# Performance work log

Measured on AMD Instinct MI355X. Metric: run time of the kernel, lower is better.

## Reference

```python
import jax, jax.numpy as jnp
import numpy as np
import math

D = 2048
NH = 16
DH = D // NH
LAT = D // 4
B, S = 2, 2048
EPS = 1e-5


def _ln(x, g, b):
    m = jnp.mean(x, axis=-1, keepdims=True)
    v = jnp.mean((x - m) ** 2, axis=-1, keepdims=True)
    return (x - m) * jax.lax.rsqrt(v + EPS) * g + b


def setup_inputs() -> dict:
    key = jax.random.key(0)
    ks = jax.random.split(key, 12)
    p = lambda k, shape: 0.01 * jax.random.normal(k, shape, dtype=jnp.float32)
    return {
        "x": jax.random.normal(ks[0], (B, S, D), dtype=jnp.float32),
        "W_dq": p(ks[1], (D, LAT)),
        "W_uq": p(ks[2], (LAT, D)),
        "q_ln_g": jnp.ones((LAT,), jnp.float32),
        "q_ln_b": jnp.zeros((LAT,), jnp.float32),
        "W_dkv": p(ks[3], (D, LAT)),
        "W_ukv": p(ks[4], (LAT, 2 * D)),
        "kv_ln_g": jnp.ones((LAT,), jnp.float32),
        "kv_ln_b": jnp.zeros((LAT,), jnp.float32),
        "W_o": p(ks[5], (D, D)),
        "norm1_g": jnp.ones((D,), jnp.float32),
        "norm1_b": jnp.zeros((D,), jnp.float32),
        "norm2_g": jnp.ones((D,), jnp.float32),
        "norm2_b": jnp.zeros((D,), jnp.float32),
        "fc1_w": p(ks[6], (4 * D, D)),
        "fc1_b": jnp.zeros((4 * D,), jnp.float32),
        "fc2_w": p(ks[7], (D, 4 * D)),
        "fc2_b": jnp.zeros((D,), jnp.float32),
    }


def reference(x, W_dq, W_uq, q_ln_g, q_ln_b, W_dkv, W_ukv, kv_ln_g, kv_ln_b,
              W_o, norm1_g, norm1_b, norm2_g, norm2_b, fc1_w, fc1_b, fc2_w, fc2_b):
    normed = _ln(x, norm1_g, norm1_b)

    # --- RopelessMLA attention ---
    cq = _ln(normed @ W_dq, q_ln_g, q_ln_b)          # [B,S,LAT]
    Q = cq @ W_uq                                     # [B,S,D]
    ckv = _ln(normed @ W_dkv, kv_ln_g, kv_ln_b)       # [B,S,LAT]
    KV = ckv @ W_ukv                                  # [B,S,2D]
    K, V = KV[..., :D], KV[..., D:]

    q = Q.reshape(B, S, NH, DH)
    k = K.reshape(B, S, NH, DH)
    v = V.reshape(B, S, NH, DH)

    qkt = jnp.einsum("bqhd,bkhd->bhqk", q, k) / math.sqrt(float(DH))
    mask = jnp.tril(jnp.ones((S, S), dtype=qkt.dtype))  # causal, past_length=0
    qkt = qkt * mask
    qkt = jnp.where(qkt == 0.0, -jnp.inf, qkt)  # faithful to original zero->-inf trick
    attn = jax.nn.softmax(qkt, axis=-1)
    o = jnp.einsum("bhqk,bkhd->bqhd", attn, v).reshape(B, S, D)
    mh_x = o @ W_o.T

    x = x + mh_x
    h = _ln(x, norm2_g, norm2_b)
    h = jax.nn.relu(h @ fc1_w.T + fc1_b)
    h = h @ fc2_w.T + fc2_b  # dropout is identity in eval mode
    return x + h
```

## Files before the change

kernel.cpp:

```cpp
#include <hip/hip_runtime.h>
#include <hip/hip_bf16.h>


#define DEVI __device__ __forceinline__

typedef __attribute__((ext_vector_type(8))) short bf16x8;
typedef __attribute__((ext_vector_type(4))) float f32x4;

DEVI unsigned short f2bf(float f) {
  union { float f; unsigned u; } v; v.f = f;
  unsigned r = v.u + 0x7fffu + ((v.u >> 16) & 1u);
  return (unsigned short)(r >> 16);
}

DEVI float bf2f(unsigned short u) {
  union { unsigned u; float f; } v; v.u = ((unsigned)u) << 16;
  return v.f;
}

#define GLDS16(gp, lp)                                              \
  __builtin_amdgcn_global_load_lds(                                 \
      (__attribute__((address_space(1))) void*)(gp),                \
      (__attribute__((address_space(3))) void*)(lp), 16, 0, 0)

#define NEG_INF (-__builtin_inff())

__global__ __launch_bounds__(256) void cast_f32_bf16(
    const float* __restrict__ in, unsigned short* __restrict__ out, long n) {
  long i = ((long)blockIdx.x * 256 + threadIdx.x) * 4;
  if (i >= n) return;
  const float4 v = *reinterpret_cast<const float4*>(in + i);
  ushort4 o;
  o.x = f2bf(v.x); o.y = f2bf(v.y); o.z = f2bf(v.z); o.w = f2bf(v.w);
  *reinterpret_cast<ushort4*>(out + i) = o;
}

__global__ __launch_bounds__(256) void transpose_cast(
    const float* __restrict__ in, unsigned short* __restrict__ out, int R, int C) {
  __shared__ float tile[32][33];
  const int c0 = blockIdx.x * 32, r0 = blockIdx.y * 32;
  const int tx = threadIdx.x & 31, ty = threadIdx.x >> 5;
#pragma unroll
  for (int i = 0; i < 32; i += 8)
    tile[ty + i][tx] = in[(long)(r0 + ty + i) * C + c0 + tx];
  __syncthreads();
#pragma unroll
  for (int i = 0; i < 32; i += 8)
    out[(long)(c0 + ty + i) * R + r0 + tx] = f2bf(tile[tx][ty + i]);
}

__global__ __launch_bounds__(256) void v_transpose(
    const unsigned short* __restrict__ KV, unsigned short* __restrict__ Vt) {
  __shared__ unsigned short sh[32][33];
  const int s0 = blockIdx.x * 32, d0 = blockIdx.y * 32, bh = blockIdx.z;
  const int b = bh >> 4, h = bh & 15;
  const int tx = threadIdx.x & 31, ty = threadIdx.x >> 5;
#pragma unroll
  for (int i = 0; i < 32; i += 8)
    sh[ty + i][tx] = KV[((long)(b * 2048 + s0 + ty + i)) * 4096 + 2048 + h * 128 + d0 + tx];
  __syncthreads();
#pragma unroll
  for (int i = 0; i < 32; i += 8)
    Vt[((long)(bh * 128 + d0 + ty + i)) * 2048 + s0 + tx] = sh[tx][ty + i];
}

DEVI float blockReduceSum(float v) {
  v += __shfl_xor(v, 1);  v += __shfl_xor(v, 2);  v += __shfl_xor(v, 4);
  v += __shfl_xor(v, 8);  v += __shfl_xor(v, 16); v += __shfl_xor(v, 32);
  __shared__ float red[4];
  if ((threadIdx.x & 63) == 0) red[threadIdx.x >> 6] = v;
  __syncthreads();
  v = red[0] + red[1] + red[2] + red[3];
  __syncthreads();
  return v;
}

template <int W>
__global__ __launch_bounds__(256) void layernorm_bf16(
    const float* __restrict__ in, const float* __restrict__ g,
    const float* __restrict__ b, unsigned short* __restrict__ out, int ldin) {
  constexpr int VPT = W / 256;
  const long row = blockIdx.x;
  const float* x = in + row * ldin;
  float v[VPT];
  float s = 0.f;
#pragma unroll
  for (int i = 0; i < VPT; i++) { v[i] = x[threadIdx.x + i * 256]; s += v[i]; }
  s = blockReduceSum(s);
  const float mean = s * (1.0f / W);
  float s2 = 0.f;
#pragma unroll
  for (int i = 0; i < VPT; i++) { float d = v[i] - mean; s2 += d * d; }
  s2 = blockReduceSum(s2);
  const float rstd = rsqrtf(s2 * (1.0f / W) + 1e-5f);
#pragma unroll
  for (int i = 0; i < VPT; i++) {
    const int c = threadIdx.x + i * 256;
    out[row * W + c] = f2bf((v[i] - mean) * rstd * g[c] + b[c]);
  }
}

__global__ __launch_bounds__(256) void combine_ln(
    const unsigned short* __restrict__ p, const float* __restrict__ xres,
    const float* __restrict__ g, const float* __restrict__ b,
    float* __restrict__ x2, unsigned short* __restrict__ h1, long n) {
  const int c0 = threadIdx.x * 8;
  const long base = (long)blockIdx.x * 2048 + c0;
  float v[8];
  float s = 0.f;
#pragma unroll
  for (int hh = 0; hh < 2; hh++) {
    const long i = base + hh * 4;
    const ushort4 a  = *reinterpret_cast<const ushort4*>(p + i);
    const ushort4 bb = *reinterpret_cast<const ushort4*>(p + n + i);
    const float4 r = *reinterpret_cast<const float4*>(xres + i);
    float4 o;
    o.x = r.x + bf2f(a.x) + bf2f(bb.x);
    o.y = r.y + bf2f(a.y) + bf2f(bb.y);
    o.z = r.z + bf2f(a.z) + bf2f(bb.z);
    o.w = r.w + bf2f(a.w) + bf2f(bb.w);
    *reinterpret_cast<float4*>(x2 + i) = o;
    v[hh * 4 + 0] = o.x; v[hh * 4 + 1] = o.y;
    v[hh * 4 + 2] = o.z; v[hh * 4 + 3] = o.w;
    s += o.x + o.y + o.z + o.w;
  }
  s = blockReduceSum(s);
  const float mean = s * (1.0f / 2048.f);
  float s2 = 0.f;
#pragma unroll
  for (int i = 0; i < 8; i++) { float d = v[i] - mean; s2 += d * d; }
  s2 = blockReduceSum(s2);
  const float rstd = rsqrtf(s2 * (1.0f / 2048.f) + 1e-5f);
#pragma unroll
  for (int hh = 0; hh < 2; hh++) {
    const float4 gv = *reinterpret_cast<const float4*>(g + c0 + hh * 4);
    const float4 bv = *reinterpret_cast<const float4*>(b + c0 + hh * 4);
    ushort4 o;
    o.x = f2bf((v[hh * 4 + 0] - mean) * rstd * gv.x + bv.x);
    o.y = f2bf((v[hh * 4 + 1] - mean) * rstd * gv.y + bv.y);
    o.z = f2bf((v[hh * 4 + 2] - mean) * rstd * gv.z + bv.z);
    o.w = f2bf((v[hh * 4 + 3] - mean) * rstd * gv.w + bv.w);
    *reinterpret_cast<ushort4*>(h1 + base + hh * 4) = o;
  }
}

template <bool BIAS, bool RELU, bool RES, bool OBF16>
__global__ __launch_bounds__(256) void gemm_bt(
    const unsigned short* __restrict__ A, const unsigned short* __restrict__ Bt,
    const float* __restrict__ bias, const float* __restrict__ res,
    void* __restrict__ Cout, int M, int N, int K) {
  __shared__ __align__(16) unsigned short As[2][128 * 32];
  __shared__ __align__(16) unsigned short Bs[2][128 * 32];

  const int m0 = blockIdx.x * 128;
  const int n0 = blockIdx.y * 128;
  const int tid = threadIdx.x;
  const int lane = tid & 63, w = tid >> 6;
  const int wr = (w >> 1) * 64, wc = (w & 1) * 64;
  const int lrow = lane & 15, lk = (lane >> 4) * 8;

  f32x4 acc[4][4] = {};

  const int nt = K >> 5;
  const int r_ = (tid * 8) >> 5;
  const int c_ = (tid * 8) & 31;

#define STAGE(buf, t)                                                        \
  {                                                                          \
    const long k0 = (long)(t) * 32;                                          \
    GLDS16(A + (long)(m0 + r_) * K + k0 + c_, &As[buf][tid * 8]);            \
    GLDS16(A + (long)(m0 + 64 + r_) * K + k0 + c_, &As[buf][2048 + tid * 8]);\
    GLDS16(Bt + (long)(n0 + r_) * K + k0 + c_, &Bs[buf][tid * 8]);           \
    GLDS16(Bt + (long)(n0 + 64 + r_) * K + k0 + c_, &Bs[buf][2048 + tid * 8]);\
  }

  STAGE(0, 0)
  __syncthreads();
  int cur = 0;
  for (int t = 0; t < nt; t++) {
    if (t + 1 < nt) STAGE(cur ^ 1, t + 1)
    bf16x8 fa[4], fb[4];
#pragma unroll
    for (int i = 0; i < 4; i++) {
      fa[i] = *reinterpret_cast<const bf16x8*>(&As[cur][(wr + i * 16 + lrow) * 32 + lk]);
      fb[i] = *reinterpret_cast<const bf16x8*>(&Bs[cur][(wc + i * 16 + lrow) * 32 + lk]);
    }
#pragma unroll
    for (int i = 0; i < 4; i++)
#pragma unroll
      for (int j = 0; j < 4; j++)
        acc[i][j] = __builtin_amdgcn_mfma_f32_16x16x32_bf16(fa[i], fb[j], acc[i][j], 0, 0, 0);
    __syncthreads();
    cur ^= 1;
  }
#undef STAGE

#pragma unroll
  for (int i = 0; i < 4; i++) {
#pragma unroll
    for (int j = 0; j < 4; j++) {
      const int row = m0 + wr + i * 16 + ((lane >> 4) << 2);
      const int col = n0 + wc + j * 16 + lrow;
      float bv = 0.f;
      if (BIAS) bv = bias[col];
#pragma unroll
      for (int r = 0; r < 4; r++) {
        float v = acc[i][j][r];
        const long idx = (long)(row + r) * N + col;
        if (BIAS) v += bv;
        if (RELU) v = fmaxf(v, 0.f);
        if (RES) v += res[idx];
        if (OBF16) ((unsigned short*)Cout)[idx] = f2bf(v);
        else       ((float*)Cout)[idx] = v;
      }
    }
  }
}

template <bool BIAS, bool RELU, bool OBF16>
__global__ __launch_bounds__(512, 1) void gemm256p(
    const unsigned short* __restrict__ A, const unsigned short* __restrict__ Bt,
    const float* __restrict__ bias, void* __restrict__ Cout,
    int M, int N, int lda, int ldb, int kLen, long kOff) {
  __shared__ __align__(16) unsigned short L[2][2][2][256 * 32];

  const int m0 = blockIdx.x * 256, n0 = blockIdx.y * 256;
  const long ka = (long)blockIdx.z * kOff;
  const int tid = threadIdx.x;
  const int lane = tid & 63, w = tid >> 6;
  const int sr = (w >> 2) * 64, sc = (w & 3) * 32;
  const int g = lane >> 4, lrow = lane & 15;
  const int r_ = tid >> 2, s_ = tid & 3;

  f32x4 acc[2][2][4][2] = {};
  const int nt = kLen >> 6;

#define STG1(bb, ab, h, kh, t, P, base0, ld)                                   \
  {                                                                            \
    const long k0 = ka + (long)(t) * 64 + (kh) * 32;                           \
    const int rr = (h) * 128 + r_;                                             \
    GLDS16((P) + (long)((base0) + rr) * (ld) + k0 + ((s_ ^ ((rr >> 1) & 3)) << 3), \
           &L[bb][ab][kh][((h) * 512 + tid) * 8]);                             \
  }
#define STG_A(bb, h, t) STG1(bb, 0, h, 0, t, A, m0, lda) STG1(bb, 0, h, 1, t, A, m0, lda)
#define STG_B(bb, h, t) STG1(bb, 1, h, 0, t, Bt, n0, ldb) STG1(bb, 1, h, 1, t, Bt, n0, ldb)

#define RD(dst, ab, kh, row)                                                   \
  dst = *reinterpret_cast<const bf16x8*>(                                      \
      &L[bu][ab][kh][((row) * 4 + (g ^ (((row) >> 1) & 3))) * 8]);

#define PH_READS(a, b)                                                         \
  bf16x8 fa[2][4], fb[2][2];                                                   \
  _Pragma("unroll")                                                            \
  for (int kh = 0; kh < 2; kh++) {                                             \
    _Pragma("unroll")                                                          \
    for (int i = 0; i < 4; i++) {                                              \
      const int rr = (a) * 128 + sr + i * 16 + lrow;                           \
      RD(fa[kh][i], 0, kh, rr)                                                 \
    }                                                                          \
    _Pragma("unroll")                                                          \
    for (int j = 0; j < 2; j++) {                                              \
      const int rr = (b) * 128 + sc + j * 16 + lrow;                           \
      RD(fb[kh][j], 1, kh, rr)                                                 \
    }                                                                          \
  }

#define PH_MFMA(a, b)                                                          \
  __builtin_amdgcn_s_setprio(1);                                               \
  _Pragma("unroll")                                                            \
  for (int kh = 0; kh < 2; kh++)                                               \
    _Pragma("unroll")                                                          \
    for (int i = 0; i < 4; i++)                                                \
      _Pragma("unroll")                                                        \
      for (int j = 0; j < 2; j++)                                              \
        acc[a][b][i][j] = __builtin_amdgcn_mfma_f32_16x16x32_bf16(             \
            fa[kh][i], fb[kh][j], acc[a][b][i][j], 0, 0, 0);                   \
  __builtin_amdgcn_s_setprio(0);

  STG_A(0, 0, 0) STG_B(0, 0, 0) STG_A(0, 1, 0) STG_B(0, 1, 0)
  asm volatile("s_waitcnt vmcnt(0)\n\ts_barrier" ::: "memory");

  int t = 0;
  for (; t < nt - 1; t++) {
    const int bu = t & 1, bn = bu ^ 1;
    {
      PH_READS(0, 0)
      STG_A(bn, 0, t + 1)
      PH_MFMA(0, 0)
      asm volatile("s_waitcnt vmcnt(4)\n\ts_barrier" ::: "memory");
    }
    {
      PH_READS(1, 0)
      STG_B(bn, 0, t + 1)
      PH_MFMA(1, 0)
      asm volatile("s_waitcnt vmcnt(4)\n\ts_barrier" ::: "memory");
    }
    {
      PH_READS(1, 1)
      STG_A(bn, 1, t + 1)
      PH_MFMA(1, 1)
    }
    {
      PH_READS(0, 1)
      STG_B(bn, 1, t + 1)
      PH_MFMA(0, 1)
      asm volatile("s_waitcnt vmcnt(4)\n\ts_barrier" ::: "memory");
    }
  }
  {
    const int bu = t & 1;
    {
      PH_READS(0, 0)
      PH_MFMA(0, 0)
      asm volatile("s_waitcnt vmcnt(2)\n\ts_barrier" ::: "memory");
    }
    {
      PH_READS(1, 0)
      PH_MFMA(1, 0)
      asm volatile("s_waitcnt vmcnt(0)\n\ts_barrier" ::: "memory");
    }
    {
      PH_READS(1, 1)
      PH_MFMA(1, 1)
    }
    {
      PH_READS(0, 1)
      PH_MFMA(0, 1)
    }
  }
#undef STG1
#undef STG_A
#undef STG_B
#undef RD
#undef PH_READS
#undef PH_MFMA

  const long zoff = (long)blockIdx.z * (long)M * (long)N;
#pragma unroll
  for (int a = 0; a < 2; a++) {
#pragma unroll
    for (int b = 0; b < 2; b++) {
#pragma unroll
      for (int i = 0; i < 4; i++) {
#pragma unroll
        for (int j = 0; j < 2; j++) {
          const int row = m0 + a * 128 + sr + i * 16 + g * 4;
          const int col = n0 + b * 128 + sc + j * 16 + lrow;
          float bv = 0.f;
          if (BIAS) bv = bias[col];
#pragma unroll
          for (int r = 0; r < 4; r++) {
            float v = acc[a][b][i][j][r];
            if (BIAS) v += bv;
            if (RELU) v = fmaxf(v, 0.f);
            const long idx = zoff + (long)(row + r) * N + col;
            if (OBF16) ((unsigned short*)Cout)[idx] = f2bf(v);
            else       ((float*)Cout)[idx] = v;
          }
        }
      }
    }
  }
}

template <bool BIAS>
__global__ __launch_bounds__(256) void combine2(
    const unsigned short* __restrict__ p, const float* __restrict__ bias,
    const float* __restrict__ res, float* __restrict__ out, long n) {
  const long i = ((long)blockIdx.x * 256 + threadIdx.x) * 4;
  if (i >= n) return;
  const ushort4 a = *reinterpret_cast<const ushort4*>(p + i);
  const ushort4 b = *reinterpret_cast<const ushort4*>(p + n + i);
  const float4 r = *reinterpret_cast<const float4*>(res + i);
  float4 o;
  o.x = bf2f(a.x) + bf2f(b.x) + r.x;
  o.y = bf2f(a.y) + bf2f(b.y) + r.y;
  o.z = bf2f(a.z) + bf2f(b.z) + r.z;
  o.w = bf2f(a.w) + bf2f(b.w) + r.w;
  if (BIAS) {
    const int col = (int)(i & 2047);
    const float4 bv = *reinterpret_cast<const float4*>(bias + col);
    o.x += bv.x; o.y += bv.y; o.z += bv.z; o.w += bv.w;
  }
  *reinterpret_cast<float4*>(out + i) = o;
}

__global__ __launch_bounds__(256) void flash_attn(
    const unsigned short* __restrict__ Q, const unsigned short* __restrict__ KV,
    const unsigned short* __restrict__ Vt, unsigned short* __restrict__ O) {
  constexpr int S = 2048;
  const int tid = threadIdx.x, lane = tid & 63, w = tid >> 6;
  const int g = lane >> 4, lcol = lane & 15;
  const int wg = blockIdx.x;
  const int x8 = wg & 7, q64 = wg >> 3;
  const int p = q64 & 15, hi = q64 >> 4;
  const int bh = x8 * 4 + hi;
  const int b = bh >> 4, h = bh & 15;
  const long kvrow0 = (long)b * S;
  const int hd0 = h * 128;

  __shared__ __align__(16) unsigned short Kl[64 * 128];
  __shared__ __align__(16) unsigned short Vl[128 * 64];
  __shared__ __align__(16) unsigned short Pl[4 * 16 * 72];

  const float kscale = 0.08838834764831845f * 1.4426950408889634f;

  for (int ti = 0; ti < 2; ti++) {
    const int t = ti ? (31 - p) : p;
    const int qbase = t * 64;
    bf16x8 qf[4];
#pragma unroll
    for (int dc = 0; dc < 4; dc++)
      qf[dc] = *reinterpret_cast<const bf16x8*>(
          Q + (kvrow0 + qbase + w * 16 + lcol) * 2048 + hd0 + dc * 32 + g * 8);
    f32x4 oacc[8] = {};
    float mst[4] = {NEG_INF, NEG_INF, NEG_INF, NEG_INF};
    float lst[4] = {0.f, 0.f, 0.f, 0.f};
    const int nk = t + 1;
    for (int kt = 0; kt < nk; kt++) {
      const int kv0 = kt * 64;
      __syncthreads();
#pragma unroll
      for (int i = 0; i < 4; i++) {
        const int o16 = i * 256 + tid;
        const int kr = o16 >> 4, ks = o16 & 15;
        GLDS16(KV + (kvrow0 + kv0 + kr) * 4096 + hd0 + 8 * (ks ^ (kr & 7)),
               Kl + o16 * 8);
        const int vd = o16 >> 3, vs = o16 & 7;
        GLDS16(Vt + ((long)bh * 128 + vd) * 2048 + kv0 + 8 * (vs ^ (vd & 7)),
               Vl + o16 * 8);
      }
      __syncthreads();
      f32x4 sc[4] = {};
      __builtin_amdgcn_s_setprio(1);
#pragma unroll
      for (int dc = 0; dc < 4; dc++) {
#pragma unroll
        for (int c = 0; c < 4; c++) {
          const bf16x8 kf = *reinterpret_cast<const bf16x8*>(
              Kl + (c * 16 + lcol) * 128 + 8 * ((4 * dc + g) ^ (lcol & 7)));
          sc[c] = __builtin_amdgcn_mfma_f32_16x16x32_bf16(qf[dc], kf, sc[c], 0, 0, 0);
        }
      }
      __builtin_amdgcn_s_setprio(0);
      float s[4][4];
      const int qrow = qbase + w * 16 + g * 4;
      if (kt == nk - 1) {
#pragma unroll
        for (int c = 0; c < 4; c++) {
          const int col = kv0 + c * 16 + lcol;
#pragma unroll
          for (int r = 0; r < 4; r++)
            s[c][r] = (col <= qrow + r) ? sc[c][r] * kscale : NEG_INF;
        }
      } else {
#pragma unroll
        for (int c = 0; c < 4; c++)
#pragma unroll
          for (int r = 0; r < 4; r++) s[c][r] = sc[c][r] * kscale;
      }
      float pm[4];
#pragma unroll
      for (int r = 0; r < 4; r++) {
        float mx = fmaxf(fmaxf(s[0][r], s[1][r]), fmaxf(s[2][r], s[3][r]));
        mx = fmaxf(mx, __shfl_xor(mx, 1));
        mx = fmaxf(mx, __shfl_xor(mx, 2));
        mx = fmaxf(mx, __shfl_xor(mx, 4));
        mx = fmaxf(mx, __shfl_xor(mx, 8));
        pm[r] = mx;
      }
      bool need = false;
#pragma unroll
      for (int r = 0; r < 4; r++) need = need || (pm[r] > mst[r] + 11.5f);
      if (__any(need)) {
#pragma unroll
        for (int r = 0; r < 4; r++) {
          const float mnew = fmaxf(mst[r], pm[r]);
          const float corr = exp2f(mst[r] - mnew);
          mst[r] = mnew;
          lst[r] *= corr;
#pragma unroll
          for (int db = 0; db < 8; db++) oacc[db][r] *= corr;
        }
      }
#pragma unroll
      for (int r = 0; r < 4; r++) {
        float ps = 0.f;
#pragma unroll
        for (int c = 0; c < 4; c++) {
          const float pv = exp2f(s[c][r] - mst[r]);
          Pl[(w * 16 + g * 4 + r) * 72 + c * 16 + lcol] = f2bf(pv);
          ps += pv;
        }
        ps += __shfl_xor(ps, 1); ps += __shfl_xor(ps, 2);
        ps += __shfl_xor(ps, 4); ps += __shfl_xor(ps, 8);
        lst[r] += ps;
      }
      __builtin_amdgcn_s_setprio(1);
#pragma unroll
      for (int kk = 0; kk < 2; kk++) {
        const bf16x8 pf = *reinterpret_cast<const bf16x8*>(
            Pl + (w * 16 + lcol) * 72 + kk * 32 + g * 8);
#pragma unroll
        for (int db = 0; db < 8; db++) {
          const bf16x8 vf = *reinterpret_cast<const bf16x8*>(
              Vl + (db * 16 + lcol) * 64 + 8 * ((4 * kk + g) ^ (lcol & 7)));
          oacc[db] = __builtin_amdgcn_mfma_f32_16x16x32_bf16(pf, vf, oacc[db], 0, 0, 0);
        }
      }
      __builtin_amdgcn_s_setprio(0);
    }
#pragma unroll
    for (int db = 0; db < 8; db++)
#pragma unroll
      for (int r = 0; r < 4; r++) {
        const int qi = qbase + w * 16 + g * 4 + r;
        O[(kvrow0 + qi) * 2048 + hd0 + db * 16 + lcol] = f2bf(oacc[db][r] / lst[r]);
      }
  }
}

extern "C" void kernel_launch(void* const* d_in, const int* in_sizes, int n_in,
                              void* d_out, int out_size, void* d_ws, size_t ws_size,
                              hipStream_t stream) {
  (void)in_sizes; (void)n_in; (void)out_size; (void)ws_size;
  const float* x     = (const float*)d_in[0];
  const float* W_dq  = (const float*)d_in[1];
  const float* W_uq  = (const float*)d_in[2];
  const float* qlng  = (const float*)d_in[3];
  const float* qlnb  = (const float*)d_in[4];
  const float* W_dkv = (const float*)d_in[5];
  const float* W_ukv = (const float*)d_in[6];
  const float* klng  = (const float*)d_in[7];
  const float* klnb  = (const float*)d_in[8];
  const float* W_o   = (const float*)d_in[9];
  const float* n1g   = (const float*)d_in[10];
  const float* n1b   = (const float*)d_in[11];
  const float* n2g   = (const float*)d_in[12];
  const float* n2b   = (const float*)d_in[13];
  const float* fc1w  = (const float*)d_in[14];
  const float* fc1b  = (const float*)d_in[15];
  const float* fc2w  = (const float*)d_in[16];
  const float* fc2b  = (const float*)d_in[17];
  float* out = (float*)d_out;

  char* ws = (char*)d_ws;
  unsigned short* normed = (unsigned short*)(ws + 0);
  unsigned short* Obuf   = (unsigned short*)(ws + 0);
  unsigned short* fc2bb  = (unsigned short*)(ws + 0);
  float*          cqkv_pre = (float*)(ws + 33554432);
  unsigned short* KV       = (unsigned short*)(ws + 33554432);
  unsigned short* fc1bb    = (unsigned short*)(ws + 33554432);
  unsigned short* fc2part  = (unsigned short*)(ws + 33554432);
  unsigned short* cq  = (unsigned short*)(ws + 67108864);
  unsigned short* Qb = (unsigned short*)(ws + 71303168);
  unsigned short* h1 = (unsigned short*)(ws + 71303168);
  unsigned short* ckv = (unsigned short*)(ws + 88080384);
  float* x2           = (float*)(ws + 88080384);
  unsigned short* Vtb    = (unsigned short*)(ws + 121634816);
  unsigned short* wopart = (unsigned short*)(ws + 121634816);
  unsigned short* hmid   = (unsigned short*)(ws + 121634816);
  unsigned short* dqkv_t = (unsigned short*)(ws + 188743680);
  unsigned short* uq_t   = dqkv_t + 2097152;
  unsigned short* ukv_t  = uq_t + 1048576;
  unsigned short* wo_b   = ukv_t + 2097152;

  const dim3 blk(256);
  const dim3 blk8(512);

  transpose_cast<<<dim3(512 / 32, 2048 / 32), blk, 0, stream>>>(W_dq, dqkv_t, 2048, 512);
  transpose_cast<<<dim3(512 / 32, 2048 / 32), blk, 0, stream>>>(W_dkv, dqkv_t + 512 * 2048, 2048, 512);
  transpose_cast<<<dim3(2048 / 32, 512 / 32), blk, 0, stream>>>(W_uq, uq_t, 512, 2048);
  transpose_cast<<<dim3(4096 / 32, 512 / 32), blk, 0, stream>>>(W_ukv, ukv_t, 512, 4096);
  cast_f32_bf16<<<2048 * 2048 / 1024, blk, 0, stream>>>(W_o, wo_b, 2048 * 2048);

  layernorm_bf16<2048><<<4096, blk, 0, stream>>>(x, n1g, n1b, normed, 2048);
  gemm_bt<false, false, false, false><<<dim3(32, 8), blk, 0, stream>>>(
      normed, dqkv_t, nullptr, nullptr, cqkv_pre, 4096, 1024, 2048);
  layernorm_bf16<512><<<4096, blk, 0, stream>>>(cqkv_pre, qlng, qlnb, cq, 1024);
  layernorm_bf16<512><<<4096, blk, 0, stream>>>(cqkv_pre + 512, klng, klnb, ckv, 1024);
  gemm_bt<false, false, false, true><<<dim3(32, 16), blk, 0, stream>>>(
      cq, uq_t, nullptr, nullptr, Qb, 4096, 2048, 512);
  gemm256p<false, false, true><<<dim3(16, 16), blk8, 0, stream>>>(
      ckv, ukv_t, nullptr, KV, 4096, 4096, 512, 512, 512, 0);
  v_transpose<<<dim3(64, 4, 32), blk, 0, stream>>>(KV, Vtb);
  flash_attn<<<dim3(512), blk, 0, stream>>>(Qb, KV, Vtb, Obuf);
  cast_f32_bf16<<<8192 * 2048 / 1024, blk, 0, stream>>>(fc1w, fc1bb, 8192L * 2048);
  gemm256p<false, false, true><<<dim3(16, 8, 2), blk8, 0, stream>>>(
      Obuf, wo_b, nullptr, wopart, 4096, 2048, 2048, 2048, 1024, 1024);
  cast_f32_bf16<<<2048 * 8192 / 1024, blk, 0, stream>>>(fc2w, fc2bb, 2048L * 8192);
  combine_ln<<<4096, blk, 0, stream>>>(wopart, x, n2g, n2b, x2, h1, 8388608L);
  gemm256p<true, true, true><<<dim3(16, 32), blk8, 0, stream>>>(
      h1, fc1bb, fc1b, hmid, 4096, 8192, 2048, 2048, 2048, 0);
  gemm256p<false, false, true><<<dim3(16, 8, 2), blk8, 0, stream>>>(
      hmid, fc2bb, nullptr, fc2part, 4096, 2048, 8192, 8192, 4096, 4096);
  combine2<true><<<8192, blk, 0, stream>>>(fc2part, fc2b, x2, out, 8388608L);
}
```

Before: 572.1 us.

## Switch 256x256 GEMM to 32x32x16 MFMA with contiguous per-wave tiles

Replaces the 16x16x32 MFMA tiling in the 256x256 GEMM with 32x32x16 MFMA. Each wave now owns a contiguous 128x64 output region rather than four scattered quadrants. The four-phase pipeline becomes two k-half phases per tile, each staging the next tile's A and B together. The aim is fewer LDS fragment reads per flop and fewer MFMA issues. In exchange there are fewer barriers per tile for overlapping loads with compute, and the epilogue writes in a different pattern.

```diff
diff --git a/kernel.cpp b/kernel.cpp
--- a/kernel.cpp
+++ b/kernel.cpp
@@ -6,6 +6,7 @@
 
 typedef __attribute__((ext_vector_type(8))) short bf16x8;
 typedef __attribute__((ext_vector_type(4))) float f32x4;
+typedef __attribute__((ext_vector_type(16))) float f32x16;
 
 DEVI unsigned short f2bf(float f) {
   union { float f; unsigned u; } v; v.f = f;
@@ -228,11 +229,11 @@
   const long ka = (long)blockIdx.z * kOff;
   const int tid = threadIdx.x;
   const int lane = tid & 63, w = tid >> 6;
-  const int sr = (w >> 2) * 64, sc = (w & 3) * 32;
-  const int g = lane >> 4, lrow = lane & 15;
+  const int wm = w >> 2, wn = w & 3;
+  const int l31 = lane & 31, khi = lane >> 5;
   const int r_ = tid >> 2, s_ = tid & 3;
 
-  f32x4 acc[2][2][4][2] = {};
+  f32x16 acc[4][2] = {};
   const int nt = kLen >> 6;
 
 #define STG1(bb, ab, h, kh, t, P, base0, ld)                                   \
@@ -242,122 +243,85 @@
     GLDS16((P) + (long)((base0) + rr) * (ld) + k0 + ((s_ ^ ((rr >> 1) & 3)) << 3), \
            &L[bb][ab][kh][((h) * 512 + tid) * 8]);                             \
   }
-#define STG_A(bb, h, t) STG1(bb, 0, h, 0, t, A, m0, lda) STG1(bb, 0, h, 1, t, A, m0, lda)
-#define STG_B(bb, h, t) STG1(bb, 1, h, 0, t, Bt, n0, ldb) STG1(bb, 1, h, 1, t, Bt, n0, ldb)
-
-#define RD(dst, ab, kh, row)                                                   \
-  dst = *reinterpret_cast<const bf16x8*>(                                      \
-      &L[bu][ab][kh][((row) * 4 + (g ^ (((row) >> 1) & 3))) * 8]);
-
-#define PH_READS(a, b)                                                         \
-  bf16x8 fa[2][4], fb[2][2];                                                   \
+#define STG_A(bb, kh, t) STG1(bb, 0, 0, kh, t, A, m0, lda) STG1(bb, 0, 1, kh, t, A, m0, lda)
+#define STG_B(bb, kh, t) STG1(bb, 1, 0, kh, t, Bt, n0, ldb) STG1(bb, 1, 1, kh, t, Bt, n0, ldb)
+
+#define PH_READS(bu, kh)                                                       \
+  bf16x8 fa[4][2], fbp[2][2];                                                  \
   _Pragma("unroll")                                                            \
-  for (int kh = 0; kh < 2; kh++) {                                             \
+  for (int i = 0; i < 4; i++) {                                                \
+    const int rr = wm * 128 + i * 32 + l31;                                    \
+    const int sw = (rr >> 1) & 3;                                              \
     _Pragma("unroll")                                                          \
-    for (int i = 0; i < 4; i++) {                                              \
-      const int rr = (a) * 128 + sr + i * 16 + lrow;                           \
-      RD(fa[kh][i], 0, kh, rr)                                                 \
-    }                                                                          \
+    for (int ks = 0; ks < 2; ks++)                                             \
+      fa[i][ks] = *reinterpret_cast<const bf16x8*>(                            \
+          &L[bu][0][kh][(rr * 4 + ((ks * 2 + khi) ^ sw)) * 8]);                \
+  }                                                                            \
+  _Pragma("unroll")                                                            \
+  for (int j = 0; j < 2; j++) {                                                \
+    const int rc = wn * 64 + j * 32 + l31;                                     \
+    const int sw = (rc >> 1) & 3;                                              \
     _Pragma("unroll")                                                          \
-    for (int j = 0; j < 2; j++) {                                              \
-      const int rr = (b) * 128 + sc + j * 16 + lrow;                           \
-      RD(fb[kh][j], 1, kh, rr)                                                 \
-    }                                                                          \
-  }
-
-#define PH_MFMA(a, b)                                                          \
+    for (int ks = 0; ks < 2; ks++)                                             \
+      fbp[j][ks] = *reinterpret_cast<const bf16x8*>(                           \
+          &L[bu][1][kh][(rc * 4 + ((ks * 2 + khi) ^ sw)) * 8]);                \
+  }
+
+#define PH_MFMA                                                                \
   __builtin_amdgcn_s_setprio(1);                                               \
   _Pragma("unroll")                                                            \
-  for (int kh = 0; kh < 2; kh++)                                               \
+  for (int ks = 0; ks < 2; ks++)                                               \
     _Pragma("unroll")                                                          \
     for (int i = 0; i < 4; i++)                                                \
       _Pragma("unroll")                                                        \
       for (int j = 0; j < 2; j++)                                              \
-        acc[a][b][i][j] = __builtin_amdgcn_mfma_f32_16x16x32_bf16(             \
-            fa[kh][i], fb[kh][j], acc[a][b][i][j], 0, 0, 0);                   \
+        acc[i][j] = __builtin_amdgcn_mfma_f32_32x32x16_bf16(                   \
+            fa[i][ks], fbp[j][ks], acc[i][j], 0, 0, 0);                        \
   __builtin_amdgcn_s_setprio(0);
 
   STG_A(0, 0, 0) STG_B(0, 0, 0) STG_A(0, 1, 0) STG_B(0, 1, 0)
   asm volatile("s_waitcnt vmcnt(0)\n\ts_barrier" ::: "memory");
 
-  int t = 0;
-  for (; t < nt - 1; t++) {
+  for (int t = 0; t < nt; t++) {
     const int bu = t & 1, bn = bu ^ 1;
+    const bool pf = (t + 1 < nt);
     {
-      PH_READS(0, 0)
-      STG_A(bn, 0, t + 1)
-      PH_MFMA(0, 0)
-      asm volatile("s_waitcnt vmcnt(4)\n\ts_barrier" ::: "memory");
+      PH_READS(bu, 0)
+      if (pf) { STG_A(bn, 0, t + 1) STG_B(bn, 0, t + 1) }
+      PH_MFMA
+      if (pf) asm volatile("s_waitcnt vmcnt(4)\n\ts_barrier" ::: "memory");
+      else    asm volatile("s_waitcnt vmcnt(0)\n\ts_barrier" ::: "memory");
     }
     {
-      PH_READS(1, 0)
-      STG_B(bn, 0, t + 1)
-      PH_MFMA(1, 0)
-      asm volatile("s_waitcnt vmcnt(4)\n\ts_barrier" ::: "memory");
-    }
-    {
-      PH_READS(1, 1)
-      STG_A(bn, 1, t + 1)
-      PH_MFMA(1, 1)
-    }
-    {
-      PH_READS(0, 1)
-      STG_B(bn, 1, t + 1)
-      PH_MFMA(0, 1)
-      asm volatile("s_waitcnt vmcnt(4)\n\ts_barrier" ::: "memory");
-    }
-  }
-  {
-    const int bu = t & 1;
-    {
-      PH_READS(0, 0)
-      PH_MFMA(0, 0)
-      asm volatile("s_waitcnt vmcnt(2)\n\ts_barrier" ::: "memory");
-    }
-    {
-      PH_READS(1, 0)
-      PH_MFMA(1, 0)
-      asm volatile("s_waitcnt vmcnt(0)\n\ts_barrier" ::: "memory");
-    }
-    {
-      PH_READS(1, 1)
-      PH_MFMA(1, 1)
-    }
-    {
-      PH_READS(0, 1)
-      PH_MFMA(0, 1)
+      PH_READS(bu, 1)
+      if (pf) { STG_A(bn, 1, t + 1) STG_B(bn, 1, t + 1) }
+      PH_MFMA
+      if (pf) asm volatile("s_waitcnt vmcnt(4)\n\ts_barrier" ::: "memory");
     }
   }
 #undef STG1
 #undef STG_A
 #undef STG_B
-#undef RD
 #undef PH_READS
 #undef PH_MFMA
 
   const long zoff = (long)blockIdx.z * (long)M * (long)N;
 #pragma unroll
-  for (int a = 0; a < 2; a++) {
-#pragma unroll
-    for (int b = 0; b < 2; b++) {
-#pragma unroll
-      for (int i = 0; i < 4; i++) {
-#pragma unroll
-        for (int j = 0; j < 2; j++) {
-          const int row = m0 + a * 128 + sr + i * 16 + g * 4;
-          const int col = n0 + b * 128 + sc + j * 16 + lrow;
-          float bv = 0.f;
-          if (BIAS) bv = bias[col];
-#pragma unroll
-          for (int r = 0; r < 4; r++) {
-            float v = acc[a][b][i][j][r];
-            if (BIAS) v += bv;
-            if (RELU) v = fmaxf(v, 0.f);
-            const long idx = zoff + (long)(row + r) * N + col;
-            if (OBF16) ((unsigned short*)Cout)[idx] = f2bf(v);
-            else       ((float*)Cout)[idx] = v;
-          }
-        }
+  for (int i = 0; i < 4; i++) {
+#pragma unroll
+    for (int j = 0; j < 2; j++) {
+      const int col = n0 + wn * 64 + j * 32 + l31;
+      float bv = 0.f;
+      if (BIAS) bv = bias[col];
+#pragma unroll
+      for (int reg = 0; reg < 16; reg++) {
+        const int row = m0 + wm * 128 + i * 32 + (reg & 3) + 8 * (reg >> 2) + 4 * khi;
+        float v = acc[i][j][reg];
+        if (BIAS) v += bv;
+        if (RELU) v = fmaxf(v, 0.f);
+        const long idx = zoff + (long)row * N + col;
+        if (OBF16) ((unsigned short*)Cout)[idx] = f2bf(v);
+        else       ((float*)Cout)[idx] = v;
       }
     }
   }
```

Result: slower. 614.2 us (+7.4%).

## Reorder GEMM phases to reuse LDS fragments and drop peeled tail

Applied to the files above, without the earlier changes.

Reorders the four sub-tile MFMA phases of the bf16 GEMM main loop to (0,0),(0,1),(1,1),(1,0). This lets A fragments be kept in registers across two phases and only B fragments be re-read, cutting LDS read traffic per K-step. The peeled last iteration is folded into the loop behind a prefetch predicate. It also cuts the number of waitcnt/barrier points per iteration from three to two and moves them. This changes how far global-to-LDS prefetch overlaps compute, and the new waitcnt counts must still guarantee buffer readiness.

```diff
diff --git a/kernel.cpp b/kernel.cpp
--- a/kernel.cpp
+++ b/kernel.cpp
@@ -245,25 +245,24 @@
 #define STG_A(bb, h, t) STG1(bb, 0, h, 0, t, A, m0, lda) STG1(bb, 0, h, 1, t, A, m0, lda)
 #define STG_B(bb, h, t) STG1(bb, 1, h, 0, t, Bt, n0, ldb) STG1(bb, 1, h, 1, t, Bt, n0, ldb)
 
-#define RD(dst, ab, kh, row)                                                   \
-  dst = *reinterpret_cast<const bf16x8*>(                                      \
-      &L[bu][ab][kh][((row) * 4 + (g ^ (((row) >> 1) & 3))) * 8]);
-
-#define PH_READS(a, b)                                                         \
-  bf16x8 fa[2][4], fb[2][2];                                                   \
+#define RD_A(fa, bu, a)                                                        \
   _Pragma("unroll")                                                            \
-  for (int kh = 0; kh < 2; kh++) {                                             \
+  for (int kh = 0; kh < 2; kh++)                                               \
     _Pragma("unroll")                                                          \
     for (int i = 0; i < 4; i++) {                                              \
       const int rr = (a) * 128 + sr + i * 16 + lrow;                           \
-      RD(fa[kh][i], 0, kh, rr)                                                 \
-    }                                                                          \
+      fa[kh][i] = *reinterpret_cast<const bf16x8*>(                            \
+          &L[bu][0][kh][(rr * 4 + (g ^ ((rr >> 1) & 3))) * 8]);                \
+    }
+#define RD_B(fb, bu, b)                                                        \
+  _Pragma("unroll")                                                            \
+  for (int kh = 0; kh < 2; kh++)                                               \
     _Pragma("unroll")                                                          \
     for (int j = 0; j < 2; j++) {                                              \
       const int rr = (b) * 128 + sc + j * 16 + lrow;                           \
-      RD(fb[kh][j], 1, kh, rr)                                                 \
-    }                                                                          \
-  }
+      fb[kh][j] = *reinterpret_cast<const bf16x8*>(                            \
+          &L[bu][1][kh][(rr * 4 + (g ^ ((rr >> 1) & 3))) * 8]);                \
+    }
 
 #define PH_MFMA(a, b)                                                          \
   __builtin_amdgcn_s_setprio(1);                                               \
@@ -277,62 +276,35 @@
             fa[kh][i], fb[kh][j], acc[a][b][i][j], 0, 0, 0);                   \
   __builtin_amdgcn_s_setprio(0);
 
-  STG_A(0, 0, 0) STG_B(0, 0, 0) STG_A(0, 1, 0) STG_B(0, 1, 0)
+  STG_A(0, 0, 0) STG_B(0, 0, 0) STG_B(0, 1, 0) STG_A(0, 1, 0)
   asm volatile("s_waitcnt vmcnt(0)\n\ts_barrier" ::: "memory");
 
-  int t = 0;
-  for (; t < nt - 1; t++) {
+  for (int t = 0; t < nt; t++) {
     const int bu = t & 1, bn = bu ^ 1;
-    {
-      PH_READS(0, 0)
-      STG_A(bn, 0, t + 1)
-      PH_MFMA(0, 0)
-      asm volatile("s_waitcnt vmcnt(4)\n\ts_barrier" ::: "memory");
-    }
-    {
-      PH_READS(1, 0)
-      STG_B(bn, 0, t + 1)
-      PH_MFMA(1, 0)
-      asm volatile("s_waitcnt vmcnt(4)\n\ts_barrier" ::: "memory");
-    }
-    {
-      PH_READS(1, 1)
-      STG_A(bn, 1, t + 1)
-      PH_MFMA(1, 1)
-    }
-    {
-      PH_READS(0, 1)
-      STG_B(bn, 1, t + 1)
-      PH_MFMA(0, 1)
-      asm volatile("s_waitcnt vmcnt(4)\n\ts_barrier" ::: "memory");
-    }
-  }
-  {
-    const int bu = t & 1;
-    {
-      PH_READS(0, 0)
-      PH_MFMA(0, 0)
-      asm volatile("s_waitcnt vmcnt(2)\n\ts_barrier" ::: "memory");
-    }
-    {
-      PH_READS(1, 0)
-      PH_MFMA(1, 0)
-      asm volatile("s_waitcnt vmcnt(0)\n\ts_barrier" ::: "memory");
-    }
-    {
-      PH_READS(1, 1)
-      PH_MFMA(1, 1)
-    }
-    {
-      PH_READS(0, 1)
-      PH_MFMA(0, 1)
-    }
+    const bool pf = (t + 1 < nt);
+    bf16x8 fa[2][4], fb[2][2];
+    RD_A(fa, bu, 0)
+    RD_B(fb, bu, 0)
+    if (pf) STG_A(bn, 0, t + 1)
+    PH_MFMA(0, 0)
+    RD_B(fb, bu, 1)
+    if (pf) STG_B(bn, 1, t + 1)
+    PH_MFMA(0, 1)
+    if (pf) asm volatile("s_waitcnt vmcnt(4)\n\ts_barrier" ::: "memory");
+    else    asm volatile("s_waitcnt vmcnt(0)\n\ts_barrier" ::: "memory");
+    RD_A(fa, bu, 1)
+    if (pf) STG_B(bn, 0, t + 1)
+    PH_MFMA(1, 1)
+    RD_B(fb, bu, 0)
+    if (pf) STG_A(bn, 1, t + 1)
+    PH_MFMA(1, 0)
+    if (pf) asm volatile("s_waitcnt vmcnt(2)\n\ts_barrier" ::: "memory");
   }
 #undef STG1
 #undef STG_A
 #undef STG_B
-#undef RD
-#undef PH_READS
+#undef RD_A
+#undef RD_B
 #undef PH_MFMA
 
   const long zoff = (long)blockIdx.z * (long)M * (long)N;
```

After: 560.6 us. 1.02x faster.
